# Kernel optimization log

Measured on AMD Instinct MI355X. Metric: run time of the kernel, lower is better.

The kernel has to match this reference:

```python
import jax, jax.numpy as jnp
import numpy as np

STRIDE = 1
PADDING = 3
DILATION = 1


def setup_inputs() -> dict:
    key = jax.random.key(0)
    k1, k2 = jax.random.split(key)
    B, C, H, W = 8, 512, 64, 64
    G, K = 8, 7
    Ho, Wo = H // STRIDE, W // STRIDE
    x = jax.random.normal(k1, (B, C, H, W), dtype=jnp.float32)
    weight = jax.random.normal(k2, (B, G, K, K, Ho, Wo), dtype=jnp.float32)
    return {"x": x, "weight": weight}


def reference(x, weight):
    # x: [B, C, H, W]; weight: [B, G, K, K, Ho, Wo]
    B, C, H, W = x.shape
    _, G, K, _, Ho, Wo = weight.shape
    cpg = C // G  # channels per group
    # zero-pad spatial dims (matches CUDA boundary check)
    xp = jnp.pad(x, ((0, 0), (0, 0), (PADDING, PADDING), (PADDING, PADDING)))
    out = jnp.zeros((B, G, cpg, Ho, Wo), dtype=x.dtype)
    for kh in range(K):
        for kw in range(K):
            h0 = kh * DILATION
            w0 = kw * DILATION
            # strided window: input pixel h*stride - pad + kh*dil for each output h
            patch = xp[:, :,
                       h0:h0 + (Ho - 1) * STRIDE + 1:STRIDE,
                       w0:w0 + (Wo - 1) * STRIDE + 1:STRIDE]  # [B, C, Ho, Wo]
            wk = weight[:, :, kh, kw]  # [B, G, Ho, Wo]
            out = out + patch.reshape(B, G, cpg, Ho, Wo) * wk[:, :, None]
    return out.reshape(B, C, Ho, Wo)
```

## Files before the change

### kernel.cpp

```cpp
#include <hip/hip_runtime.h>


#define BB 8
#define CC 512
#define GG 8
#define CPG 64
#define HH 64
#define WW 64
#define HW (HH * WW)
#define KK 7
#define PAD 3

#define TILE_ROWS 8
#define CSPLIT 2
#define NCHUNK 4
#define CHPC 8
#define LDS_ROWS (TILE_ROWS + KK - 1)
#define LDS_PITCH 72
#define CH_STRIDE (LDS_ROWS * LDS_PITCH)
#define NQUADS (LDS_ROWS * (LDS_PITCH / 4))

__global__ __launch_bounds__(256, 4)
void involution_kernel(const float* __restrict__ x,
                       const float* __restrict__ weight,
                       float* __restrict__ out) {
    const int tid = threadIdx.x;
    const int tx = tid & 31;
    const int ty = tid >> 5;
    const int bx = blockIdx.x;
    const int tile = bx >> 1;
    const int cs = bx & 1;
    const int g = blockIdx.y;
    const int b = blockIdx.z;

    const int wo0 = tx << 1;
    const int hbase = tile * TILE_ROWS;
    const int ho = hbase + ty;

    __shared__ float xs[CHPC * CH_STRIDE];

    const float* wq = weight + ((size_t)(b * GG + g) * (KK * KK)) * HW
                    + ho * WW + wo0;

    const int sr = tid / 18;
    const int sq = tid - sr * 18;
    const int xrow = hbase + sr - PAD;
    const int xcol = sq * 4 - 4;
    const bool sval = (tid < NQUADS)
                   && ((unsigned)xrow < HH) && ((unsigned)xcol < WW);
    const int soff = xrow * WW + xcol;
    const int ldsoff = sr * LDS_PITCH + sq * 4;

    const size_t cbase = (size_t)(b * CC + g * CPG + cs * (NCHUNK * CHPC)) * HW;
    const float* xg = x + cbase;
    float* og = out + cbase + ho * WW + wo0;

#pragma unroll 1
    for (int cc = 0; cc < NCHUNK; ++cc) {
        float4 q[CHPC];
#pragma unroll
        for (int ch = 0; ch < CHPC; ++ch) {
            float4 v = make_float4(0.f, 0.f, 0.f, 0.f);
            if (sval)
                v = *(const float4*)(xg + (size_t)(cc * CHPC + ch) * HW + soff);
            q[ch] = v;
        }
        __syncthreads();
        if (tid < NQUADS) {
#pragma unroll
            for (int ch = 0; ch < CHPC; ++ch)
                *(float4*)(&xs[ch * CH_STRIDE + ldsoff]) = q[ch];
        }
        __syncthreads();

        float acc0[CHPC], acc1[CHPC];
#pragma unroll
        for (int ch = 0; ch < CHPC; ++ch) { acc0[ch] = 0.f; acc1[ch] = 0.f; }

#pragma unroll
        for (int kh = 0; kh < KK; ++kh) {
            float2 wk[KK];
#pragma unroll
            for (int j = 0; j < KK; ++j)
                wk[j] = *(const float2*)(wq + (size_t)(kh * KK + j) * HW);

#pragma unroll
            for (int ch = 0; ch < CHPC; ++ch) {
                const float* row = &xs[ch * CH_STRIDE + (ty + kh) * LDS_PITCH + wo0];
                const float2 p0 = *(const float2*)(row + 0);
                const float2 p1 = *(const float2*)(row + 2);
                const float2 p2 = *(const float2*)(row + 4);
                const float2 p3 = *(const float2*)(row + 6);
                const float2 p4 = *(const float2*)(row + 8);
                const float f1 = p0.y, f2 = p1.x, f3 = p1.y, f4 = p2.x;
                const float f5 = p2.y, f6 = p3.x, f7 = p3.y, f8 = p4.x;
                float a0 = acc0[ch], a1 = acc1[ch];
                a0 = fmaf(f1, wk[0].x, a0);  a1 = fmaf(f2, wk[0].y, a1);
                a0 = fmaf(f2, wk[1].x, a0);  a1 = fmaf(f3, wk[1].y, a1);
                a0 = fmaf(f3, wk[2].x, a0);  a1 = fmaf(f4, wk[2].y, a1);
                a0 = fmaf(f4, wk[3].x, a0);  a1 = fmaf(f5, wk[3].y, a1);
                a0 = fmaf(f5, wk[4].x, a0);  a1 = fmaf(f6, wk[4].y, a1);
                a0 = fmaf(f6, wk[5].x, a0);  a1 = fmaf(f7, wk[5].y, a1);
                a0 = fmaf(f7, wk[6].x, a0);  a1 = fmaf(f8, wk[6].y, a1);
                acc0[ch] = a0; acc1[ch] = a1;
            }
        }

#pragma unroll
        for (int ch = 0; ch < CHPC; ++ch) {
            *(float2*)(og + (size_t)(cc * CHPC + ch) * HW)
                = make_float2(acc0[ch], acc1[ch]);
        }
    }
}

extern "C" void kernel_launch(void* const* d_in, const int* in_sizes, int n_in,
                              void* d_out, int out_size, void* d_ws, size_t ws_size,
                              hipStream_t stream) {
    const float* x = (const float*)d_in[0];
    const float* w = (const float*)d_in[1];
    float* out = (float*)d_out;

    dim3 grid((HH / TILE_ROWS) * CSPLIT, GG, BB);
    dim3 block(256);
    involution_kernel<<<grid, block, 0, stream>>>(x, w, out);
}
```

Baseline: 202.3 us.

## Software-pipeline x chunk loads and double-buffer weight row loads

Hoists the first chunk's global x loads before the loop and prefetches the next chunk's x into registers right after the LDS store, so global latency overlaps the FMA work. Weight rows are double-buffered across kh steps, with the next row loaded while the current one is consumed. This raises register pressure (extra float4 q[8] and float2 wkb[7] live across compute) under launch_bounds(256,4), which may cause spills or lower occupancy.

```diff
diff --git a/kernel.cpp b/kernel.cpp
--- a/kernel.cpp
+++ b/kernel.cpp
@@ -55,17 +55,23 @@
     const float* xg = x + cbase;
     float* og = out + cbase + ho * WW + wo0;
 
+    float4 q[CHPC];
+#pragma unroll
+    for (int ch = 0; ch < CHPC; ++ch) {
+        float4 v = make_float4(0.f, 0.f, 0.f, 0.f);
+        if (sval)
+            v = *(const float4*)(xg + (size_t)ch * HW + soff);
+        q[ch] = v;
+    }
+    float2 wka[KK], wkb[KK];
+#pragma unroll
+    for (int j = 0; j < KK; ++j)
+        wka[j] = *(const float2*)(wq + (size_t)j * HW);
+
 #pragma unroll 1
     for (int cc = 0; cc < NCHUNK; ++cc) {
-        float4 q[CHPC];
-#pragma unroll
-        for (int ch = 0; ch < CHPC; ++ch) {
-            float4 v = make_float4(0.f, 0.f, 0.f, 0.f);
-            if (sval)
-                v = *(const float4*)(xg + (size_t)(cc * CHPC + ch) * HW + soff);
-            q[ch] = v;
-        }
-        __syncthreads();
+        asm volatile("" ::: "memory");
+        if (cc) __syncthreads();
         if (tid < NQUADS) {
 #pragma unroll
             for (int ch = 0; ch < CHPC; ++ch)
@@ -73,38 +79,58 @@
         }
         __syncthreads();
 
+        if (cc + 1 < NCHUNK) {
+#pragma unroll
+            for (int ch = 0; ch < CHPC; ++ch) {
+                float4 v = make_float4(0.f, 0.f, 0.f, 0.f);
+                if (sval)
+                    v = *(const float4*)(xg + (size_t)((cc + 1) * CHPC + ch) * HW + soff);
+                q[ch] = v;
+            }
+        }
+
         float acc0[CHPC], acc1[CHPC];
 #pragma unroll
         for (int ch = 0; ch < CHPC; ++ch) { acc0[ch] = 0.f; acc1[ch] = 0.f; }
 
-#pragma unroll
-        for (int kh = 0; kh < KK; ++kh) {
-            float2 wk[KK];
-#pragma unroll
-            for (int j = 0; j < KK; ++j)
-                wk[j] = *(const float2*)(wq + (size_t)(kh * KK + j) * HW);
+#define KH_STEP(KH, WCUR, WNXT, NKH)                                        \
+        {                                                                   \
+            _Pragma("unroll")                                               \
+            for (int j = 0; j < KK; ++j)                                    \
+                WNXT[j] = *(const float2*)(wq + (size_t)((NKH) * KK + j) * HW); \
+            _Pragma("unroll")                                               \
+            for (int ch = 0; ch < CHPC; ++ch) {                             \
+                const float* row = &xs[ch * CH_STRIDE + (ty + (KH)) * LDS_PITCH + wo0]; \
+                const float2 p0 = *(const float2*)(row + 0);                \
+                const float2 p1 = *(const float2*)(row + 2);                \
+                const float2 p2 = *(const float2*)(row + 4);                \
+                const float2 p3 = *(const float2*)(row + 6);                \
+                const float2 p4 = *(const float2*)(row + 8);                \
+                const float f1 = p0.y, f2 = p1.x, f3 = p1.y, f4 = p2.x;     \
+                const float f5 = p2.y, f6 = p3.x, f7 = p3.y, f8 = p4.x;     \
+                float a0 = acc0[ch], a1 = acc1[ch];                         \
+                a0 = fmaf(f1, WCUR[0].x, a0);  a1 = fmaf(f2, WCUR[0].y, a1); \
+                a0 = fmaf(f2, WCUR[1].x, a0);  a1 = fmaf(f3, WCUR[1].y, a1); \
+                a0 = fmaf(f3, WCUR[2].x, a0);  a1 = fmaf(f4, WCUR[2].y, a1); \
+                a0 = fmaf(f4, WCUR[3].x, a0);  a1 = fmaf(f5, WCUR[3].y, a1); \
+                a0 = fmaf(f5, WCUR[4].x, a0);  a1 = fmaf(f6, WCUR[4].y, a1); \
+                a0 = fmaf(f6, WCUR[5].x, a0);  a1 = fmaf(f7, WCUR[5].y, a1); \
+                a0 = fmaf(f7, WCUR[6].x, a0);  a1 = fmaf(f8, WCUR[6].y, a1); \
+                acc0[ch] = a0; acc1[ch] = a1;                               \
+            }                                                               \
+        }
+
+        KH_STEP(0, wka, wkb, 1)
+        KH_STEP(1, wkb, wka, 2)
+        KH_STEP(2, wka, wkb, 3)
+        KH_STEP(3, wkb, wka, 4)
+        KH_STEP(4, wka, wkb, 5)
+        KH_STEP(5, wkb, wka, 6)
+        KH_STEP(6, wka, wkb, 0)
+#undef KH_STEP
 
 #pragma unroll
-            for (int ch = 0; ch < CHPC; ++ch) {
-                const float* row = &xs[ch * CH_STRIDE + (ty + kh) * LDS_PITCH + wo0];
-                const float2 p0 = *(const float2*)(row + 0);
-                const float2 p1 = *(const float2*)(row + 2);
-                const float2 p2 = *(const float2*)(row + 4);
-                const float2 p3 = *(const float2*)(row + 6);
-                const float2 p4 = *(const float2*)(row + 8);
-                const float f1 = p0.y, f2 = p1.x, f3 = p1.y, f4 = p2.x;
-                const float f5 = p2.y, f6 = p3.x, f7 = p3.y, f8 = p4.x;
-                float a0 = acc0[ch], a1 = acc1[ch];
-                a0 = fmaf(f1, wk[0].x, a0);  a1 = fmaf(f2, wk[0].y, a1);
-                a0 = fmaf(f2, wk[1].x, a0);  a1 = fmaf(f3, wk[1].y, a1);
-                a0 = fmaf(f3, wk[2].x, a0);  a1 = fmaf(f4, wk[2].y, a1);
-                a0 = fmaf(f4, wk[3].x, a0);  a1 = fmaf(f5, wk[3].y, a1);
-                a0 = fmaf(f5, wk[4].x, a0);  a1 = fmaf(f6, wk[4].y, a1);
-                a0 = fmaf(f6, wk[5].x, a0);  a1 = fmaf(f7, wk[5].y, a1);
-                a0 = fmaf(f7, wk[6].x, a0);  a1 = fmaf(f8, wk[6].y, a1);
-                acc0[ch] = a0; acc1[ch] = a1;
-            }
-        }
+        for (int j = 0; j < KK; ++j) wka[j] = wkb[j];
 
 #pragma unroll
         for (int ch = 0; ch < CHPC; ++ch) {
```

New measurement: 270.8 us. 33.8% more time.
